# Performance work log

Hardware: AMD Instinct MI355X
Metric: run time of the kernel (lower is better)

The kernel has to match this reference:

```python
import jax, jax.numpy as jnp
import numpy as np

# ---- static config (mirrors DescriptorModule init args) ----
S, N = 8, 2048                 # n_snap, n_points
ATOM_TYPES = [0, 1]
MAX_NEIGHS = [24, 40]          # per neighbor-type slot counts
CUM = [0, 24, 64]              # cumulative neighbor offsets
T = 64                         # total_num_neighs
D_HID, D_EMB = 32, 64          # descrip_dim = [1, 32, 64]
SUB = 16                       # dim_sub_net
LENGTH = 1.0                   # periodic box length
R_CS, R_C = 0.3, 0.6           # smooth cutoff radii
# net id for (atom_type i, neighbor_type k): pairs 00->0, 01->1, 11->2
PAIR_IDX = np.array([[0, 1], [1, 2]], dtype=np.int64)


def setup_inputs() -> dict:
    key = jax.random.key(0)
    ks = jax.random.split(key, 8)
    inputs = jax.random.uniform(ks[0], (S, N, 3), dtype=jnp.float32)
    input_types = jax.random.randint(ks[1], (1, N), 0, 2)
    # avoid self-neighbors (zero distance): offset in [1, N)
    offs = jax.random.randint(ks[2], (S, N, T), 1, N)
    neigh_list = (jnp.arange(N, dtype=jnp.int64)[None, :, None] + offs) % N
    # per-type-pair MLP params, stacked on leading pair axis (3 pairs)
    W1 = jax.random.normal(ks[3], (3, 1, D_HID), dtype=jnp.float32)
    b1 = 0.1 * jax.random.normal(ks[4], (3, D_HID), dtype=jnp.float32)
    W2 = jax.random.normal(ks[5], (3, D_HID, D_EMB), dtype=jnp.float32) / np.sqrt(D_HID)
    b2 = 0.1 * jax.random.normal(ks[6], (3, D_EMB), dtype=jnp.float32)
    return {"inputs": inputs, "W1": W1, "b1": b1, "W2": W2, "b2": b2,
            "input_types": input_types, "neigh_list": neigh_list}


def _descriptor(inputs, W1, b1, W2, b2, input_types, neigh_list):
    # gather neighbor coordinates: (S, N, T, 3)
    pos_n = jax.vmap(lambda p, nl: p[nl])(inputs, neigh_list)
    diff = pos_n - inputs[:, :, None, :]
    diff = diff - LENGTH * jnp.round(diff / LENGTH)          # minimum image
    dist = jnp.sqrt(jnp.sum(diff * diff, axis=-1))           # (S, N, T)
    dist = jnp.maximum(dist, jnp.asarray(1e-12, dist.dtype))
    s = 1.0 / dist
    # smooth cutoff on s(r) = 1/r
    u = (dist - R_CS) / (R_C - R_CS)
    factor = jnp.where(dist < R_CS, 1.0,
                       jnp.where(dist < R_C, 0.5 * jnp.cos(jnp.pi * u) + 0.5, 0.0))
    s = s * factor                                           # (S, N, T)
    r_ij = (diff / dist[..., None]) * s[..., None]           # (S, N, T, 3)

    # per-atom net selection: net_idx[n, k] = pair id for atom n, neighbor type k
    net_idx = jnp.asarray(PAIR_IDX)[input_types[0]]          # (N, n_types)
    g_parts = []
    for k, (a, b) in enumerate(zip(CUM[:-1], CUM[1:])):
        idx = net_idx[:, k]                                  # (N,)
        w1 = W1[idx][:, 0, :]                                # (N, H)
        h = s[:, :, a:b, None] * w1[None, :, None, :] + b1[idx][None, :, None, :]
        h = jax.nn.relu(h)                                   # (S, N, Tk, H)
        g = jnp.einsum('snkh,nhe->snke', h, W2[idx]) + b2[idx][None, :, None, :]
        g_parts.append(g)
    G = jnp.concatenate(g_parts, axis=2)                     # (S, N, T, E)

    r_tilde = jnp.concatenate([s[..., None], r_ij], axis=-1)  # (S, N, T, 4)
    G2 = G[..., :SUB]
    R = jnp.einsum('snta,snte->snae', r_tilde, G2)            # (S, N, 4, SUB)
    R1 = jnp.einsum('snta,snae->snte', r_tilde, R)            # (S, N, T, SUB)
    D = jnp.einsum('snte,sntf->snef', G, R1)                  # (S, N, E, SUB)
    return D


def reference(inputs, W1, b1, W2, b2, input_types, neigh_list):
    return _descriptor(inputs, W1, b1, W2, b2, input_types, neigh_list)
```

## Files before the change

kernel.cpp:

```cpp
#include <hip/hip_runtime.h>

namespace {
constexpr int kN   = 2048;
constexpr int kT   = 64;
constexpr int kDH  = 32;
constexpr int kDE  = 64;
constexpr int kSUB = 16;
constexpr int kCUT = 24;
constexpr int kAPB = 8;
constexpr float kRcs = 0.3f;
constexpr float kRc  = 0.6f;
constexpr float kPi  = 3.14159265358979323846f;
}

__global__ __launch_bounds__(512, 6)
void descriptor_kernel(const float* __restrict__ pos,
                       const float* __restrict__ W1,
                       const float* __restrict__ b1,
                       const float* __restrict__ W2,
                       const float* __restrict__ b2,
                       const int*   __restrict__ types,
                       const int*   __restrict__ neigh,
                       float*       __restrict__ out)
{
    __shared__ float sW2x[3][kDH + 1][kDE];
    __shared__ float sW1[3][kDH];
    __shared__ float sB1[3][kDH];
    __shared__ float sRT[kAPB][kT][4];
    __shared__ float sP[kAPB][2][kDH + 1][4];
    __shared__ float sQ[kAPB][kDE][4];

    const int tid = threadIdx.x;
    const int w = tid >> 6;
    const int q = tid & 63;

    for (int i = tid; i < 3 * kDH * kDE; i += 512) {
        const int net = i >> 11;
        const int r = i & 2047;
        sW2x[net][r >> 6][r & 63] = W2[i];
    }
    if (tid < 3 * kDE) sW2x[tid / kDE][kDH][tid % kDE] = b2[tid];
    if (tid < 3 * kDH) {
        sW1[tid / kDH][tid % kDH] = W1[tid];
        sB1[tid / kDH][tid % kDH] = b1[tid];
    }

    const int atom = blockIdx.x * kAPB + w;
    const int sidx = atom >> 11;
    const int n = atom & (kN - 1);
    const int ty = types[n];

    {
        const int t = q;
        const int j = neigh[(size_t)atom * kT + t];
        const float* pn = pos + (size_t)atom * 3;
        const float* pj = pos + ((size_t)sidx * kN + j) * 3;
        float dx = pj[0] - pn[0]; dx -= rintf(dx);
        float dy = pj[1] - pn[1]; dy -= rintf(dy);
        float dz = pj[2] - pn[2]; dz -= rintf(dz);
        float dist = sqrtf(dx * dx + dy * dy + dz * dz);
        dist = fmaxf(dist, 1e-12f);
        const float u = (dist - kRcs) * (1.0f / (kRc - kRcs));
        const float sw = 0.5f * __cosf(kPi * u) + 0.5f;
        const float factor = (dist < kRcs) ? 1.0f : ((dist < kRc) ? sw : 0.0f);
        const float sv = factor / dist;
        const float inv = sv / dist;
        *(float4*)&sRT[w][t][0] = make_float4(sv, dx * inv, dy * inv, dz * inv);
    }
    __syncthreads();

    if (q <= kDH) {
        const int hi = q;
        const bool bias = (hi == kDH);
        const int hc = bias ? 0 : hi;
        const float w10 = bias ? 0.0f : sW1[ty][hc];
        const float b10 = bias ? 1.0f : sB1[ty][hc];
        const float w11 = bias ? 0.0f : sW1[ty + 1][hc];
        const float b11 = bias ? 1.0f : sB1[ty + 1][hc];
        float a0 = 0.f, a1 = 0.f, a2 = 0.f, a3 = 0.f;
        float c0 = 0.f, c1 = 0.f, c2 = 0.f, c3 = 0.f;
        #pragma unroll 8
        for (int t = 0; t < kCUT; ++t) {
            const float4 rt = *(const float4*)&sRT[w][t][0];
            const float hv = fmaxf(fmaf(rt.x, w10, b10), 0.0f);
            a0 = fmaf(rt.x, hv, a0);
            a1 = fmaf(rt.y, hv, a1);
            a2 = fmaf(rt.z, hv, a2);
            a3 = fmaf(rt.w, hv, a3);
        }
        #pragma unroll 8
        for (int t = kCUT; t < kT; ++t) {
            const float4 rt = *(const float4*)&sRT[w][t][0];
            const float hv = fmaxf(fmaf(rt.x, w11, b11), 0.0f);
            c0 = fmaf(rt.x, hv, c0);
            c1 = fmaf(rt.y, hv, c1);
            c2 = fmaf(rt.z, hv, c2);
            c3 = fmaf(rt.w, hv, c3);
        }
        *(float4*)&sP[w][0][hi][0] = make_float4(a0, a1, a2, a3);
        *(float4*)&sP[w][1][hi][0] = make_float4(c0, c1, c2, c3);
    }
    __syncthreads();

    {
        const int e = q;
        float q0 = 0.f, q1 = 0.f, q2 = 0.f, q3 = 0.f;
        #pragma unroll
        for (int k = 0; k < 2; ++k) {
            const float (*w2n)[kDE] = sW2x[ty + k];
            #pragma unroll
            for (int hi = 0; hi <= kDH; ++hi) {
                const float wv = w2n[hi][e];
                const float4 p = *(const float4*)&sP[w][k][hi][0];
                q0 = fmaf(p.x, wv, q0);
                q1 = fmaf(p.y, wv, q1);
                q2 = fmaf(p.z, wv, q2);
                q3 = fmaf(p.w, wv, q3);
            }
        }
        *(float4*)&sQ[w][e][0] = make_float4(q0, q1, q2, q3);
    }
    __syncthreads();

    {
        const int e = q;
        const float4 qe = *(const float4*)&sQ[w][e][0];
        float4* op = (float4*)(out + ((size_t)atom * kDE + e) * kSUB);
        #pragma unroll
        for (int fq = 0; fq < 4; ++fq) {
            float rr[4];
            #pragma unroll
            for (int m = 0; m < 4; ++m) {
                const float4 qf = *(const float4*)&sQ[w][fq * 4 + m][0];
                rr[m] = qe.x * qf.x + qe.y * qf.y + qe.z * qf.z + qe.w * qf.w;
            }
            op[fq] = make_float4(rr[0], rr[1], rr[2], rr[3]);
        }
    }
}

extern "C" void kernel_launch(void* const* d_in, const int* in_sizes, int n_in,
                              void* d_out, int out_size, void* d_ws, size_t ws_size,
                              hipStream_t stream)
{
    (void)in_sizes; (void)n_in; (void)out_size; (void)d_ws; (void)ws_size;
    const float* pos   = (const float*)d_in[0];
    const float* W1    = (const float*)d_in[1];
    const float* b1    = (const float*)d_in[2];
    const float* W2    = (const float*)d_in[3];
    const float* b2    = (const float*)d_in[4];
    const int*   types = (const int*)d_in[5];
    const int*   neigh = (const int*)d_in[6];
    float* out = (float*)d_out;

    const int total_atoms = 8 * kN;
    dim3 grid(total_atoms / kAPB), block(512);
    hipLaunchKernelGGL(descriptor_kernel, grid, block, 0, stream,
                       pos, W1, b1, W2, b2, types, neigh, out);
}
```

Baseline: 120.6 us.

## Replace shared-memory staging with wavefront readlane broadcasts and paired W2 table

Per-atom intermediates (neighbor features, per-hidden projections, Q rows) now stay in registers and are broadcast across the wavefront with readlane, instead of being written to and read back from LDS. Two of the three block-wide barriers are removed. W2 and b2 are repacked into an interleaved float2 table per atom type, so one LDS load feeds both networks. Occupancy hint raised to 8. The trade-off is many scalar readlane instructions (SALU/VALU dependency) and full unrolling across 64 neighbors, which increases instruction count and register pressure.

```diff
diff --git a/kernel.cpp b/kernel.cpp
--- a/kernel.cpp
+++ b/kernel.cpp
@@ -13,43 +13,48 @@
 constexpr float kPi  = 3.14159265358979323846f;
 }
 
-__global__ __launch_bounds__(512, 6)
+__device__ __forceinline__ float rlane(float v, int lane) {
+    return __int_as_float(__builtin_amdgcn_readlane(__float_as_int(v), lane));
+}
+
+__global__ __launch_bounds__(512, 8)
 void descriptor_kernel(const float* __restrict__ pos,
-                       const float* __restrict__ W1,
-                       const float* __restrict__ b1,
-                       const float* __restrict__ W2,
-                       const float* __restrict__ b2,
+                       const float* __restrict__ gW1,
+                       const float* __restrict__ gB1,
+                       const float* __restrict__ gW2,
+                       const float* __restrict__ gB2,
                        const int*   __restrict__ types,
                        const int*   __restrict__ neigh,
                        float*       __restrict__ out)
 {
-    __shared__ float sW2x[3][kDH + 1][kDE];
-    __shared__ float sW1[3][kDH];
-    __shared__ float sB1[3][kDH];
-    __shared__ float sRT[kAPB][kT][4];
-    __shared__ float sP[kAPB][2][kDH + 1][4];
-    __shared__ float sQ[kAPB][kDE][4];
+    __shared__ float2 sPair[2][kDH + 1][kDE];
 
     const int tid = threadIdx.x;
+
+    for (int i = tid; i < 2 * (kDH + 1) * kDE; i += 512) {
+        const int ty = i / ((kDH + 1) * kDE);
+        const int r  = i % ((kDH + 1) * kDE);
+        const int hi = r / kDE;
+        const int e  = r % kDE;
+        float a, c;
+        if (hi < kDH) {
+            a = gW2[ty * (kDH * kDE) + hi * kDE + e];
+            c = gW2[(ty + 1) * (kDH * kDE) + hi * kDE + e];
+        } else {
+            a = gB2[ty * kDE + e];
+            c = gB2[(ty + 1) * kDE + e];
+        }
+        sPair[ty][hi][e] = make_float2(a, c);
+    }
+
     const int w = tid >> 6;
     const int q = tid & 63;
-
-    for (int i = tid; i < 3 * kDH * kDE; i += 512) {
-        const int net = i >> 11;
-        const int r = i & 2047;
-        sW2x[net][r >> 6][r & 63] = W2[i];
-    }
-    if (tid < 3 * kDE) sW2x[tid / kDE][kDH][tid % kDE] = b2[tid];
-    if (tid < 3 * kDH) {
-        sW1[tid / kDH][tid % kDH] = W1[tid];
-        sB1[tid / kDH][tid % kDH] = b1[tid];
-    }
-
     const int atom = blockIdx.x * kAPB + w;
     const int sidx = atom >> 11;
     const int n = atom & (kN - 1);
     const int ty = types[n];
 
+    float vS, vX, vY, vZ;
     {
         const int t = q;
         const int j = neigh[(size_t)atom * kT + t];
@@ -63,78 +68,80 @@
         const float u = (dist - kRcs) * (1.0f / (kRc - kRcs));
         const float sw = 0.5f * __cosf(kPi * u) + 0.5f;
         const float factor = (dist < kRcs) ? 1.0f : ((dist < kRc) ? sw : 0.0f);
-        const float sv = factor / dist;
-        const float inv = sv / dist;
-        *(float4*)&sRT[w][t][0] = make_float4(sv, dx * inv, dy * inv, dz * inv);
+        vS = factor / dist;
+        const float inv = vS / dist;
+        vX = dx * inv; vY = dy * inv; vZ = dz * inv;
     }
+
+    const int hc = (q < kDH) ? q : 0;
+    float w1A = gW1[ty * kDH + hc];
+    float b1A = gB1[ty * kDH + hc];
+    float w1B = gW1[(ty + 1) * kDH + hc];
+    float b1B = gB1[(ty + 1) * kDH + hc];
+    if (q >= kDH) { w1A = 0.0f; b1A = 1.0f; w1B = 0.0f; b1B = 1.0f; }
+
+    float P00 = 0.f, P01 = 0.f, P02 = 0.f, P03 = 0.f;
+    float P10 = 0.f, P11 = 0.f, P12 = 0.f, P13 = 0.f;
+    #pragma unroll
+    for (int t = 0; t < kT; ++t) {
+        const float sx = rlane(vS, t);
+        const float xx = rlane(vX, t);
+        const float yy = rlane(vY, t);
+        const float zz = rlane(vZ, t);
+        if (t < kCUT) {
+            const float h = fmaxf(fmaf(sx, w1A, b1A), 0.0f);
+            P00 = fmaf(sx, h, P00);
+            P01 = fmaf(xx, h, P01);
+            P02 = fmaf(yy, h, P02);
+            P03 = fmaf(zz, h, P03);
+        } else {
+            const float h = fmaxf(fmaf(sx, w1B, b1B), 0.0f);
+            P10 = fmaf(sx, h, P10);
+            P11 = fmaf(xx, h, P11);
+            P12 = fmaf(yy, h, P12);
+            P13 = fmaf(zz, h, P13);
+        }
+    }
+
     __syncthreads();
 
-    if (q <= kDH) {
-        const int hi = q;
-        const bool bias = (hi == kDH);
-        const int hc = bias ? 0 : hi;
-        const float w10 = bias ? 0.0f : sW1[ty][hc];
-        const float b10 = bias ? 1.0f : sB1[ty][hc];
-        const float w11 = bias ? 0.0f : sW1[ty + 1][hc];
-        const float b11 = bias ? 1.0f : sB1[ty + 1][hc];
-        float a0 = 0.f, a1 = 0.f, a2 = 0.f, a3 = 0.f;
-        float c0 = 0.f, c1 = 0.f, c2 = 0.f, c3 = 0.f;
-        #pragma unroll 8
-        for (int t = 0; t < kCUT; ++t) {
-            const float4 rt = *(const float4*)&sRT[w][t][0];
-            const float hv = fmaxf(fmaf(rt.x, w10, b10), 0.0f);
-            a0 = fmaf(rt.x, hv, a0);
-            a1 = fmaf(rt.y, hv, a1);
-            a2 = fmaf(rt.z, hv, a2);
-            a3 = fmaf(rt.w, hv, a3);
+    float q0 = 0.f, q1 = 0.f, q2 = 0.f, q3 = 0.f;
+    {
+        const int e = q;
+        #pragma unroll
+        for (int hi = 0; hi <= kDH; ++hi) {
+            const float2 wv = sPair[ty][hi][e];
+            const float s0 = rlane(P00, hi), s1 = rlane(P01, hi);
+            const float s2 = rlane(P02, hi), s3 = rlane(P03, hi);
+            const float u0 = rlane(P10, hi), u1 = rlane(P11, hi);
+            const float u2 = rlane(P12, hi), u3 = rlane(P13, hi);
+            q0 = fmaf(s0, wv.x, q0);
+            q1 = fmaf(s1, wv.x, q1);
+            q2 = fmaf(s2, wv.x, q2);
+            q3 = fmaf(s3, wv.x, q3);
+            q0 = fmaf(u0, wv.y, q0);
+            q1 = fmaf(u1, wv.y, q1);
+            q2 = fmaf(u2, wv.y, q2);
+            q3 = fmaf(u3, wv.y, q3);
         }
-        #pragma unroll 8
-        for (int t = kCUT; t < kT; ++t) {
-            const float4 rt = *(const float4*)&sRT[w][t][0];
-            const float hv = fmaxf(fmaf(rt.x, w11, b11), 0.0f);
-            c0 = fmaf(rt.x, hv, c0);
-            c1 = fmaf(rt.y, hv, c1);
-            c2 = fmaf(rt.z, hv, c2);
-            c3 = fmaf(rt.w, hv, c3);
-        }
-        *(float4*)&sP[w][0][hi][0] = make_float4(a0, a1, a2, a3);
-        *(float4*)&sP[w][1][hi][0] = make_float4(c0, c1, c2, c3);
     }
-    __syncthreads();
 
     {
         const int e = q;
-        float q0 = 0.f, q1 = 0.f, q2 = 0.f, q3 = 0.f;
-        #pragma unroll
-        for (int k = 0; k < 2; ++k) {
-            const float (*w2n)[kDE] = sW2x[ty + k];
-            #pragma unroll
-            for (int hi = 0; hi <= kDH; ++hi) {
-                const float wv = w2n[hi][e];
-                const float4 p = *(const float4*)&sP[w][k][hi][0];
-                q0 = fmaf(p.x, wv, q0);
-                q1 = fmaf(p.y, wv, q1);
-                q2 = fmaf(p.z, wv, q2);
-                q3 = fmaf(p.w, wv, q3);
-            }
-        }
-        *(float4*)&sQ[w][e][0] = make_float4(q0, q1, q2, q3);
-    }
-    __syncthreads();
-
-    {
-        const int e = q;
-        const float4 qe = *(const float4*)&sQ[w][e][0];
         float4* op = (float4*)(out + ((size_t)atom * kDE + e) * kSUB);
         #pragma unroll
-        for (int fq = 0; fq < 4; ++fq) {
+        for (int fg = 0; fg < 4; ++fg) {
             float rr[4];
             #pragma unroll
             for (int m = 0; m < 4; ++m) {
-                const float4 qf = *(const float4*)&sQ[w][fq * 4 + m][0];
-                rr[m] = qe.x * qf.x + qe.y * qf.y + qe.z * qf.z + qe.w * qf.w;
+                const int f = fg * 4 + m;
+                const float a0 = rlane(q0, f);
+                const float a1 = rlane(q1, f);
+                const float a2 = rlane(q2, f);
+                const float a3 = rlane(q3, f);
+                rr[m] = fmaf(q3, a3, fmaf(q2, a2, fmaf(q1, a1, q0 * a0)));
             }
-            op[fq] = make_float4(rr[0], rr[1], rr[2], rr[3]);
+            op[fg] = make_float4(rr[0], rr[1], rr[2], rr[3]);
         }
     }
 }
```

Result: slower. 126.4 us (+4.8%).

## Move per-atom contractions onto bf16 MFMA with four atoms per wave

Applied to the files above, without the earlier changes.

Reworks the kernel so each wave handles four atoms instead of one. The r_tilde × hidden-layer contraction and the W2 projection now run as bf16 16x16x32 MFMA instructions in place of scalar FMA loops, with W2 staged transposed in LDS as bf16. This cuts the per-block weight staging overhead and the scalar FMA work, and drops two block-wide barriers. The cost is lower precision: activations and weights are rounded to bf16, which may break tolerance. It also adds complex lane masking and fragment packing.

```diff
diff --git a/kernel.cpp b/kernel.cpp
--- a/kernel.cpp
+++ b/kernel.cpp
@@ -1,60 +1,76 @@
 #include <hip/hip_runtime.h>
+#include <hip/hip_bf16.h>
+#include <string.h>
 
 namespace {
 constexpr int kN   = 2048;
 constexpr int kT   = 64;
-constexpr int kDH  = 32;
 constexpr int kDE  = 64;
 constexpr int kSUB = 16;
-constexpr int kCUT = 24;
-constexpr int kAPB = 8;
 constexpr float kRcs = 0.3f;
 constexpr float kRc  = 0.6f;
 constexpr float kPi  = 3.14159265358979323846f;
 }
 
-__global__ __launch_bounds__(512, 6)
+typedef __attribute__((ext_vector_type(8))) short bf16x8;
+typedef __attribute__((ext_vector_type(4))) float f32x4;
+
+union Frag { bf16x8 v; int i[4]; };
+
+__device__ __forceinline__ int pack2(float a, float b) {
+    __hip_bfloat162 h = __float22bfloat162_rn(make_float2(a, b));
+    int r; memcpy(&r, &h, 4); return r;
+}
+
+__global__ __launch_bounds__(512, 4)
 void descriptor_kernel(const float* __restrict__ pos,
-                       const float* __restrict__ W1,
-                       const float* __restrict__ b1,
-                       const float* __restrict__ W2,
-                       const float* __restrict__ b2,
+                       const float* __restrict__ gW1,
+                       const float* __restrict__ gB1,
+                       const float* __restrict__ gW2,
+                       const float* __restrict__ gB2,
                        const int*   __restrict__ types,
                        const int*   __restrict__ neigh,
                        float*       __restrict__ out)
 {
-    __shared__ float sW2x[3][kDH + 1][kDE];
-    __shared__ float sW1[3][kDH];
-    __shared__ float sB1[3][kDH];
-    __shared__ float sRT[kAPB][kT][4];
-    __shared__ float sP[kAPB][2][kDH + 1][4];
-    __shared__ float sQ[kAPB][kDE][4];
-
-    const int tid = threadIdx.x;
-    const int w = tid >> 6;
-    const int q = tid & 63;
-
-    for (int i = tid; i < 3 * kDH * kDE; i += 512) {
+    __shared__ short sW2t[kDE][104];
+    __shared__ float sB2[3][kDE];
+    __shared__ __align__(16) char arena[8][4][1024];
+
+    const int tid  = threadIdx.x;
+    const int w    = tid >> 6;
+    const int lane = tid & 63;
+    const int rg   = lane >> 4;
+    const int c    = lane & 15;
+
+    for (int i = tid; i < 3 * 32 * kDE; i += 512) {
         const int net = i >> 11;
-        const int r = i & 2047;
-        sW2x[net][r >> 6][r & 63] = W2[i];
-    }
-    if (tid < 3 * kDE) sW2x[tid / kDE][kDH][tid % kDE] = b2[tid];
-    if (tid < 3 * kDH) {
-        sW1[tid / kDH][tid % kDH] = W1[tid];
-        sB1[tid / kDH][tid % kDH] = b1[tid];
-    }
-
-    const int atom = blockIdx.x * kAPB + w;
-    const int sidx = atom >> 11;
-    const int n = atom & (kN - 1);
-    const int ty = types[n];
-
-    {
-        const int t = q;
-        const int j = neigh[(size_t)atom * kT + t];
+        const int hi  = (i >> 6) & 31;
+        const int e   = i & 63;
+        sW2t[e][net * 32 + hi] = (short)(pack2(gW2[i], 0.0f) & 0xFFFF);
+    }
+    if (tid < 3 * kDE) sB2[tid >> 6][tid & 63] = gB2[tid];
+
+    const bool keep0 = (((c >> 2) & 1) == ((rg == 3) ? 1 : 0));
+    const bool keep1 = (((c >> 2) & 1) == 1);
+    const int ones_pk = (c == 0) ? 0x3F803F80 : 0;
+
+    float w1v[3][2], b1v[3][2];
+    #pragma unroll
+    for (int net = 0; net < 3; ++net)
+        #pragma unroll
+        for (int hf = 0; hf < 2; ++hf) {
+            w1v[net][hf] = gW1[net * 32 + hf * 16 + c];
+            b1v[net][hf] = gB1[net * 32 + hf * 16 + c];
+        }
+
+    const int atomBase = blockIdx.x * 32 + w * 4;
+
+    #pragma unroll
+    for (int g = 0; g < 4; ++g) {
+        const int atom = atomBase + g;
+        const int j = neigh[(size_t)atom * kT + lane];
+        const float* pj = pos + ((size_t)((atom >> 11) << 11) + j) * 3;
         const float* pn = pos + (size_t)atom * 3;
-        const float* pj = pos + ((size_t)sidx * kN + j) * 3;
         float dx = pj[0] - pn[0]; dx -= rintf(dx);
         float dy = pj[1] - pn[1]; dy -= rintf(dy);
         float dz = pj[2] - pn[2]; dz -= rintf(dz);
@@ -65,76 +81,153 @@
         const float factor = (dist < kRcs) ? 1.0f : ((dist < kRc) ? sw : 0.0f);
         const float sv = factor / dist;
         const float inv = sv / dist;
-        *(float4*)&sRT[w][t][0] = make_float4(sv, dx * inv, dy * inv, dz * inv);
-    }
+        float* rt = (float*)arena[w][g];
+        rt[lane]       = sv;
+        rt[64 + lane]  = dx * inv;
+        rt[128 + lane] = dy * inv;
+        rt[192 + lane] = dz * inv;
+    }
+
+    #pragma unroll
+    for (int g = 0; g < 4; ++g) {
+        const int ty = types[(atomBase + g) & (kN - 1)];
+        const float wA0 = ty ? w1v[1][0] : w1v[0][0];
+        const float wA1 = ty ? w1v[1][1] : w1v[0][1];
+        const float bA0 = ty ? b1v[1][0] : b1v[0][0];
+        const float bA1 = ty ? b1v[1][1] : b1v[0][1];
+        const float wB0 = ty ? w1v[2][0] : w1v[1][0];
+        const float wB1 = ty ? w1v[2][1] : w1v[1][1];
+        const float bB0 = ty ? b1v[2][0] : b1v[1][0];
+        const float bB1 = ty ? b1v[2][1] : b1v[1][1];
+
+        const float* rt = (const float*)arena[w][g];
+        f32x4 acc0 = {0.f, 0.f, 0.f, 0.f};
+        f32x4 acc1 = {0.f, 0.f, 0.f, 0.f};
+        f32x4 accB = {0.f, 0.f, 0.f, 0.f};
+
+        #pragma unroll
+        for (int Ks = 0; Ks < 2; ++Ks) {
+            const int tb = Ks * 32 + rg * 8;
+            const float4 s0 = *(const float4*)(rt + tb);
+            const float4 s1 = *(const float4*)(rt + tb + 4);
+            const float4 r0 = *(const float4*)(rt + (c & 3) * 64 + tb);
+            const float4 r1 = *(const float4*)(rt + (c & 3) * 64 + tb + 4);
+            const bool kp = Ks ? keep1 : keep0;
+            Frag B;
+            B.i[0] = kp ? pack2(r0.x, r0.y) : 0;
+            B.i[1] = kp ? pack2(r0.z, r0.w) : 0;
+            B.i[2] = kp ? pack2(r1.x, r1.y) : 0;
+            B.i[3] = kp ? pack2(r1.z, r1.w) : 0;
+
+            const bool useA = (Ks == 0) && (rg < 3);
+            const float w0 = useA ? wA0 : wB0, b0 = useA ? bA0 : bB0;
+            const float w1_ = useA ? wA1 : wB1, b1_ = useA ? bA1 : bB1;
+
+            Frag A0, A1;
+            {
+                const float h0 = fmaxf(fmaf(s0.x, w0, b0), 0.f);
+                const float h1 = fmaxf(fmaf(s0.y, w0, b0), 0.f);
+                const float h2 = fmaxf(fmaf(s0.z, w0, b0), 0.f);
+                const float h3 = fmaxf(fmaf(s0.w, w0, b0), 0.f);
+                const float h4 = fmaxf(fmaf(s1.x, w0, b0), 0.f);
+                const float h5 = fmaxf(fmaf(s1.y, w0, b0), 0.f);
+                const float h6 = fmaxf(fmaf(s1.z, w0, b0), 0.f);
+                const float h7 = fmaxf(fmaf(s1.w, w0, b0), 0.f);
+                A0.i[0] = pack2(h0, h1); A0.i[1] = pack2(h2, h3);
+                A0.i[2] = pack2(h4, h5); A0.i[3] = pack2(h6, h7);
+            }
+            {
+                const float h0 = fmaxf(fmaf(s0.x, w1_, b1_), 0.f);
+                const float h1 = fmaxf(fmaf(s0.y, w1_, b1_), 0.f);
+                const float h2 = fmaxf(fmaf(s0.z, w1_, b1_), 0.f);
+                const float h3 = fmaxf(fmaf(s0.w, w1_, b1_), 0.f);
+                const float h4 = fmaxf(fmaf(s1.x, w1_, b1_), 0.f);
+                const float h5 = fmaxf(fmaf(s1.y, w1_, b1_), 0.f);
+                const float h6 = fmaxf(fmaf(s1.z, w1_, b1_), 0.f);
+                const float h7 = fmaxf(fmaf(s1.w, w1_, b1_), 0.f);
+                A1.i[0] = pack2(h0, h1); A1.i[1] = pack2(h2, h3);
+                A1.i[2] = pack2(h4, h5); A1.i[3] = pack2(h6, h7);
+            }
+            Frag Ab; Ab.i[0] = ones_pk; Ab.i[1] = ones_pk; Ab.i[2] = ones_pk; Ab.i[3] = ones_pk;
+
+            acc0 = __builtin_amdgcn_mfma_f32_16x16x32_bf16(A0.v, B.v, acc0, 0, 0, 0);
+            acc1 = __builtin_amdgcn_mfma_f32_16x16x32_bf16(A1.v, B.v, acc1, 0, 0, 0);
+            accB = __builtin_amdgcn_mfma_f32_16x16x32_bf16(Ab.v, B.v, accB, 0, 0, 0);
+        }
+
+        short* pbf = (short*)arena[w][g];
+        if (c < 8) {
+            const int kb = c >> 2, a = c & 3;
+            short* p = pbf + a * 120 + (ty + kb) * 40;
+            *(int*)(p + rg * 4)      = pack2(acc0[0], acc0[1]);
+            *(int*)(p + rg * 4 + 2)  = pack2(acc0[2], acc0[3]);
+            *(int*)(p + 16 + rg * 4)     = pack2(acc1[0], acc1[1]);
+            *(int*)(p + 16 + rg * 4 + 2) = pack2(acc1[2], acc1[3]);
+            if (rg == 0) ((float*)(arena[w][g] + 960))[kb * 4 + a] = accB[0];
+        }
+        const int netz = ty ? 0 : 2;
+        *(int*)(pbf + rg * 120 + netz * 40 + c * 2) = 0;
+    }
+
     __syncthreads();
 
-    if (q <= kDH) {
-        const int hi = q;
-        const bool bias = (hi == kDH);
-        const int hc = bias ? 0 : hi;
-        const float w10 = bias ? 0.0f : sW1[ty][hc];
-        const float b10 = bias ? 1.0f : sB1[ty][hc];
-        const float w11 = bias ? 0.0f : sW1[ty + 1][hc];
-        const float b11 = bias ? 1.0f : sB1[ty + 1][hc];
-        float a0 = 0.f, a1 = 0.f, a2 = 0.f, a3 = 0.f;
-        float c0 = 0.f, c1 = 0.f, c2 = 0.f, c3 = 0.f;
-        #pragma unroll 8
-        for (int t = 0; t < kCUT; ++t) {
-            const float4 rt = *(const float4*)&sRT[w][t][0];
-            const float hv = fmaxf(fmaf(rt.x, w10, b10), 0.0f);
-            a0 = fmaf(rt.x, hv, a0);
-            a1 = fmaf(rt.y, hv, a1);
-            a2 = fmaf(rt.z, hv, a2);
-            a3 = fmaf(rt.w, hv, a3);
-        }
-        #pragma unroll 8
-        for (int t = kCUT; t < kT; ++t) {
-            const float4 rt = *(const float4*)&sRT[w][t][0];
-            const float hv = fmaxf(fmaf(rt.x, w11, b11), 0.0f);
-            c0 = fmaf(rt.x, hv, c0);
-            c1 = fmaf(rt.y, hv, c1);
-            c2 = fmaf(rt.z, hv, c2);
-            c3 = fmaf(rt.w, hv, c3);
-        }
-        *(float4*)&sP[w][0][hi][0] = make_float4(a0, a1, a2, a3);
-        *(float4*)&sP[w][1][hi][0] = make_float4(c0, c1, c2, c3);
-    }
-    __syncthreads();
-
+    Frag A3_0, A3_1, A3_2;
     {
-        const int e = q;
-        float q0 = 0.f, q1 = 0.f, q2 = 0.f, q3 = 0.f;
-        #pragma unroll
-        for (int k = 0; k < 2; ++k) {
-            const float (*w2n)[kDE] = sW2x[ty + k];
-            #pragma unroll
-            for (int hi = 0; hi <= kDH; ++hi) {
-                const float wv = w2n[hi][e];
-                const float4 p = *(const float4*)&sP[w][k][hi][0];
-                q0 = fmaf(p.x, wv, q0);
-                q1 = fmaf(p.y, wv, q1);
-                q2 = fmaf(p.z, wv, q2);
-                q3 = fmaf(p.w, wv, q3);
-            }
-        }
-        *(float4*)&sQ[w][e][0] = make_float4(q0, q1, q2, q3);
-    }
-    __syncthreads();
-
+        const short* base = (const short*)arena[w][c >> 2] + (c & 3) * 120 + rg * 8;
+        A3_0.v = *(const bf16x8*)(base);
+        A3_1.v = *(const bf16x8*)(base + 40);
+        A3_2.v = *(const bf16x8*)(base + 80);
+    }
+    f32x4 q0 = {0.f,0.f,0.f,0.f}, q1 = {0.f,0.f,0.f,0.f};
+    f32x4 q2 = {0.f,0.f,0.f,0.f}, q3 = {0.f,0.f,0.f,0.f};
+    #pragma unroll
+    for (int Nt = 0; Nt < 4; ++Nt) {
+        const int e = Nt * 16 + c;
+        f32x4 acc = {0.f,0.f,0.f,0.f};
+        acc = __builtin_amdgcn_mfma_f32_16x16x32_bf16(A3_0.v, *(const bf16x8*)&sW2t[e][rg * 8],      acc, 0, 0, 0);
+        acc = __builtin_amdgcn_mfma_f32_16x16x32_bf16(A3_1.v, *(const bf16x8*)&sW2t[e][32 + rg * 8], acc, 0, 0, 0);
+        acc = __builtin_amdgcn_mfma_f32_16x16x32_bf16(A3_2.v, *(const bf16x8*)&sW2t[e][64 + rg * 8], acc, 0, 0, 0);
+        if (Nt == 0) q0 = acc; else if (Nt == 1) q1 = acc; else if (Nt == 2) q2 = acc; else q3 = acc;
+    }
     {
-        const int e = q;
-        const float4 qe = *(const float4*)&sQ[w][e][0];
-        float4* op = (float4*)(out + ((size_t)atom * kDE + e) * kSUB);
-        #pragma unroll
-        for (int fq = 0; fq < 4; ++fq) {
+        const int tyr = types[(atomBase + rg) & (kN - 1)];
+        #pragma unroll
+        for (int kb = 0; kb < 2; ++kb) {
+            const float4 pb = *(const float4*)(arena[w][rg] + 960 + kb * 16);
+            const float* b2row = sB2[tyr + kb];
+            const float v0 = b2row[c], v1 = b2row[16 + c], v2 = b2row[32 + c], v3 = b2row[48 + c];
+            q0[0] = fmaf(pb.x, v0, q0[0]); q0[1] = fmaf(pb.y, v0, q0[1]);
+            q0[2] = fmaf(pb.z, v0, q0[2]); q0[3] = fmaf(pb.w, v0, q0[3]);
+            q1[0] = fmaf(pb.x, v1, q1[0]); q1[1] = fmaf(pb.y, v1, q1[1]);
+            q1[2] = fmaf(pb.z, v1, q1[2]); q1[3] = fmaf(pb.w, v1, q1[3]);
+            q2[0] = fmaf(pb.x, v2, q2[0]); q2[1] = fmaf(pb.y, v2, q2[1]);
+            q2[2] = fmaf(pb.z, v2, q2[2]); q2[3] = fmaf(pb.w, v2, q2[3]);
+            q3[0] = fmaf(pb.x, v3, q3[0]); q3[1] = fmaf(pb.y, v3, q3[1]);
+            q3[2] = fmaf(pb.z, v3, q3[2]); q3[3] = fmaf(pb.w, v3, q3[3]);
+        }
+    }
+    {
+        float* qm = (float*)arena[w][rg];
+        *(f32x4*)(qm + (0 * 16 + c) * 4) = q0;
+        *(f32x4*)(qm + (1 * 16 + c) * 4) = q1;
+        *(f32x4*)(qm + (2 * 16 + c) * 4) = q2;
+        *(f32x4*)(qm + (3 * 16 + c) * 4) = q3;
+    }
+
+    #pragma unroll
+    for (int g = 0; g < 4; ++g) {
+        const float* qm = (const float*)arena[w][g];
+        const f32x4 qe = *(const f32x4*)(qm + lane * 4);
+        float* op = out + ((size_t)(atomBase + g) * kDE + lane) * kSUB;
+        #pragma unroll
+        for (int fg = 0; fg < 4; ++fg) {
             float rr[4];
             #pragma unroll
             for (int m = 0; m < 4; ++m) {
-                const float4 qf = *(const float4*)&sQ[w][fq * 4 + m][0];
-                rr[m] = qe.x * qf.x + qe.y * qf.y + qe.z * qf.z + qe.w * qf.w;
+                const f32x4 qf = *(const f32x4*)(qm + (fg * 4 + m) * 4);
+                rr[m] = fmaf(qe[3], qf[3], fmaf(qe[2], qf[2], fmaf(qe[1], qf[1], qe[0] * qf[0])));
             }
-            op[fq] = make_float4(rr[0], rr[1], rr[2], rr[3]);
+            *(float4*)(op + fg * 4) = make_float4(rr[0], rr[1], rr[2], rr[3]);
         }
     }
 }
@@ -149,12 +242,12 @@
     const float* b1    = (const float*)d_in[2];
     const float* W2    = (const float*)d_in[3];
     const float* b2    = (const float*)d_in[4];
-    const int*   types = (const int*)d_in[5];
+    const int*   typesp= (const int*)d_in[5];
     const int*   neigh = (const int*)d_in[6];
     float* out = (float*)d_out;
 
     const int total_atoms = 8 * kN;
-    dim3 grid(total_atoms / kAPB), block(512);
+    dim3 grid(total_atoms / 32), block(512);
     hipLaunchKernelGGL(descriptor_kernel, grid, block, 0, stream,
-                       pos, W1, b1, W2, b2, types, neigh, out);
-}
+                       pos, W1, b1, W2, b2, typesp, neigh, out);
+}
```

Result: faster. 114.9 us (-4.7%).
